# Performance work log

Hardware: AMD Instinct MI355X
Metric: run time of the kernel (lower is better)

Reference implementation:

```python
import jax, jax.numpy as jnp
import numpy as np

PATCH = 16       # patch_size
HALF = 8         # patch_size // 2
SEARCH_HALF = 20 # search_size // 2
NCAND = 40       # candidates per axis (stride=1)
WIN = NCAND + PATCH  # 56: search window side
NUM_PATCHES = 256
IMG_RES = 256    # hard-coded in `patch_ids * H // 256`
EPS = 1e-7


def setup_inputs() -> dict:
    key = jax.random.key(0)
    k0, k1, k2, k3, k4 = jax.random.split(key, 5)
    feat0 = jax.random.normal(k0, (1, 3, 256, 256), jnp.float32)
    feat1 = jax.random.normal(k1, (1, 256, 256, 256), jnp.float32)
    feat2 = jax.random.normal(k2, (1, 512, 128, 128), jnp.float32)
    feat3 = jax.random.normal(k3, (1, 1024, 64, 64), jnp.float32)
    # interior location so the 40x40 candidate grid is full (static shape)
    sample_loc = jax.random.randint(k4, (2,), 28, 228, dtype=jnp.int32)
    return {"feat0": feat0, "feat1": feat1, "feat2": feat2,
            "feat3": feat3, "sample_loc": sample_loc}


def _l2norm(x):
    # Normalize(power=2): x / (sqrt(sum(x^2, dim=1)) + 1e-7)
    norm = jnp.sqrt(jnp.sum(x * x, axis=1, keepdims=True))
    return x / (norm + EPS)


def _select_patch_ids(img, sample_loc):
    # brute-force SSD search of 16x16 patches in a 40x40 stride-1 grid
    C = img.shape[1]
    lh, lw = sample_loc[0], sample_loc[1]
    window = jax.lax.dynamic_slice(
        img, (0, 0, lh - SEARCH_HALF - HALF, lw - SEARCH_HALF - HALF),
        (1, C, WIN, WIN))[0]                       # [C,56,56]
    idx = jnp.arange(NCAND)[:, None] + jnp.arange(PATCH)[None, :]  # [40,16]
    # all candidate patches: [C,40,40,16,16]
    patches = window[:, idx[:, None, :, None], idx[None, :, None, :]]
    sample = jax.lax.dynamic_slice(
        img, (0, 0, lh - HALF, lw - HALF), (1, C, PATCH, PATCH))[0]  # [C,16,16]
    diff = patches - sample[:, None, None, :, :]
    dist = jnp.sqrt(jnp.sum(diff * diff, axis=(0, 3, 4)))  # [40,40] L2 distance
    # topk smallest, sorted ascending
    _, top_idx = jax.lax.top_k(-dist.reshape(-1), NUM_PATCHES)
    hs = lh - SEARCH_HALF + jnp.arange(NCAND)
    ws = lw - SEARCH_HALF + jnp.arange(NCAND)
    locs = jnp.stack(jnp.meshgrid(hs, ws, indexing='ij'), axis=-1).reshape(-1, 2)
    return locs[top_idx].astype(jnp.int32)  # [256,2]


def _gather_norm(feat, patch_ids):
    B, C, H, W = feat.shape
    feat_reshape = feat.transpose(0, 2, 3, 1).reshape(B, H * W, C)
    feat_patch_loc = (patch_ids * H) // IMG_RES          # floor_divide
    patch_id = feat_patch_loc[:, 0] * W + feat_patch_loc[:, 1]
    x_sample = feat_reshape[:, patch_id, :].reshape(-1, C)  # [B*256, C]
    return _l2norm(x_sample)


def reference(feat0, feat1, feat2, feat3, sample_loc):
    patch_ids = _select_patch_ids(feat0, sample_loc)
    outs = tuple(_gather_norm(f, patch_ids) for f in (feat0, feat1, feat2, feat3))
    return (*outs, patch_ids)
```

## Files before the change

### kernel.cpp

```cpp
#include <hip/hip_runtime.h>

#define NCAND 40
#define NC2   1600
#define NP    256

__global__ void k_dist(const float* __restrict__ feat0,
                       const int* __restrict__ loc,
                       float* __restrict__ dist) {
    __shared__ float smp[3 * 16 * 16];
    const int lh = loc[0], lw = loc[1];
    for (int t = threadIdx.x; t < 768; t += 256) {
        int c = t >> 8;
        int rem = t & 255;
        int a = rem >> 4;
        int b = rem & 15;
        smp[t] = feat0[c * 65536 + (lh - 8 + a) * 256 + (lw - 8 + b)];
    }
    __syncthreads();

    const int wid  = threadIdx.x >> 6;
    const int lane = threadIdx.x & 63;
    const int cand = blockIdx.x * 4 + wid;
    const int i = cand / NCAND;
    const int j = cand % NCAND;
    const int base_h = lh - 28 + i;
    const int base_w = lw - 28 + j;

    int c = lane >> 4;
    if (c > 2) c = 0;
    const int h = (lane >> 3) & 1;
    const int u = lane & 7;
    const float* fp = feat0 + c * 65536;
    const float* sc = smp + c * 256;

    float r = 0.0f;
#pragma unroll
    for (int k = 0; k < 16; ++k) {
        const int idx = h * 128 + k * 8 + u;
        const int a = idx >> 4;
        const int b = idx & 15;
        float v = fp[(base_h + a) * 256 + base_w + b];
        float d = __fsub_rn(v, sc[idx]);
        float sq = __fmul_rn(d, d);
        r = (k == 0) ? sq : __fadd_rn(r, sq);
    }
    r = __fadd_rn(r, __shfl_xor(r, 1, 64));
    r = __fadd_rn(r, __shfl_xor(r, 2, 64));
    r = __fadd_rn(r, __shfl_xor(r, 4, 64));
    r = __fadd_rn(r, __shfl_xor(r, 8, 64));
    float p1 = __shfl(r, 16, 64);
    float p2 = __shfl(r, 32, 64);
    float tot = __fadd_rn(__fadd_rn(r, p1), p2);
    if (lane == 0) dist[cand] = __fsqrt_rn(tot);
}

template <int C, int H>
__device__ __forceinline__ void wave_gather(const float* __restrict__ src,
                                            long off, int r, int h, int w,
                                            int lane, float* __restrict__ out) {
    const int hh = (h * H) / 256;
    const int ww = (w * H) / 256;
    const long HW = (long)H * H;
    const long base = (long)hh * H + ww;

    float x[(C + 63) / 64];
    float acc = 0.f;
#pragma unroll
    for (int m = 0; m < (C + 63) / 64; ++m) {
        const int c = lane + m * 64;
        float v = (c < C) ? src[(long)c * HW + base] : 0.f;
        x[m] = v;
        acc = fmaf(v, v, acc);
    }
    acc += __shfl_xor(acc, 1, 64);
    acc += __shfl_xor(acc, 2, 64);
    acc += __shfl_xor(acc, 4, 64);
    acc += __shfl_xor(acc, 8, 64);
    acc += __shfl_xor(acc, 16, 64);
    acc += __shfl_xor(acc, 32, 64);
    const float scale = 1.0f / (sqrtf(acc) + 1e-7f);
#pragma unroll
    for (int m = 0; m < (C + 63) / 64; ++m) {
        const int c = lane + m * 64;
        if (c < C) out[off + (long)r * C + c] = x[m] * scale;
    }
}

__global__ void k_rankgather(const float* __restrict__ dist,
                             const int* __restrict__ loc,
                             const float* __restrict__ feat0,
                             const float* __restrict__ feat1,
                             const float* __restrict__ feat2,
                             const float* __restrict__ feat3,
                             float* __restrict__ out) {
    __shared__ float ds[NC2];
    for (int k = threadIdx.x; k < NC2; k += 256) ds[k] = dist[k];
    __syncthreads();

    const int wid  = threadIdx.x >> 6;
    const int lane = threadIdx.x & 63;
    const int t = blockIdx.x * 4 + wid;
    const float dt = ds[t];
    int rank = 0;
#pragma unroll
    for (int m = 0; m < NC2 / 64; ++m) {
        const int k = lane + (m << 6);
        const float dk = ds[k];
        rank += (dk < dt || (dk == dt && k < t)) ? 1 : 0;
    }
    rank += __shfl_xor(rank, 1, 64);
    rank += __shfl_xor(rank, 2, 64);
    rank += __shfl_xor(rank, 4, 64);
    rank += __shfl_xor(rank, 8, 64);
    rank += __shfl_xor(rank, 16, 64);
    rank += __shfl_xor(rank, 32, 64);

    if (rank < NP) {
        const int lh = loc[0], lw = loc[1];
        const int h = lh - 20 + t / NCAND;
        const int w = lw - 20 + t % NCAND;
        if (lane == 0) {
            float* out_ids = out + 768 + 65536 + 131072 + 262144;
            out_ids[rank * 2]     = (float)h;
            out_ids[rank * 2 + 1] = (float)w;
        }
        wave_gather<3,    256>(feat0, 0,                      rank, h, w, lane, out);
        wave_gather<256,  256>(feat1, 768,                    rank, h, w, lane, out);
        wave_gather<512,  128>(feat2, 768 + 65536,            rank, h, w, lane, out);
        wave_gather<1024, 64 >(feat3, 768 + 65536 + 131072,   rank, h, w, lane, out);
    }
}

extern "C" void kernel_launch(void* const* d_in, const int* in_sizes, int n_in,
                              void* d_out, int out_size, void* d_ws, size_t ws_size,
                              hipStream_t stream) {
    const float* feat0 = (const float*)d_in[0];
    const float* feat1 = (const float*)d_in[1];
    const float* feat2 = (const float*)d_in[2];
    const float* feat3 = (const float*)d_in[3];
    const int*   loc   = (const int*)d_in[4];
    float* out = (float*)d_out;

    float* dist = (float*)d_ws;

    k_dist<<<NC2 / 4, 256, 0, stream>>>(feat0, loc, dist);
    k_rankgather<<<NC2 / 4, 256, 0, stream>>>(dist, loc, feat0, feat1, feat2, feat3, out);
}
```

Baseline: 19.80 us.

## Prefetch feature gathers speculatively before rank computation and drop shared-memory staging

In the rank-and-gather kernel, each wave now issues its gather loads for all four feature maps, plus the distance values, straight into registers before computing the candidate's rank. Before, those loads waited until the rank test passed. The shared-memory staging and barriers are removed from both kernels, and the sample patch is read directly from global memory. This overlaps the gather latency with the rank reduction, at the cost of roughly six times as many gathers, since all 1600 candidates load even though only 256 are kept, and higher register pressure.

```diff
diff --git a/kernel.cpp b/kernel.cpp
--- a/kernel.cpp
+++ b/kernel.cpp
@@ -7,19 +7,9 @@
 __global__ void k_dist(const float* __restrict__ feat0,
                        const int* __restrict__ loc,
                        float* __restrict__ dist) {
-    __shared__ float smp[3 * 16 * 16];
-    const int lh = loc[0], lw = loc[1];
-    for (int t = threadIdx.x; t < 768; t += 256) {
-        int c = t >> 8;
-        int rem = t & 255;
-        int a = rem >> 4;
-        int b = rem & 15;
-        smp[t] = feat0[c * 65536 + (lh - 8 + a) * 256 + (lw - 8 + b)];
-    }
-    __syncthreads();
-
     const int wid  = threadIdx.x >> 6;
     const int lane = threadIdx.x & 63;
+    const int lh = loc[0], lw = loc[1];
     const int cand = blockIdx.x * 4 + wid;
     const int i = cand / NCAND;
     const int j = cand % NCAND;
@@ -31,16 +21,20 @@
     const int h = (lane >> 3) & 1;
     const int u = lane & 7;
     const float* fp = feat0 + c * 65536;
-    const float* sc = smp + c * 256;
 
-    float r = 0.0f;
+    float v[16], s[16];
 #pragma unroll
     for (int k = 0; k < 16; ++k) {
         const int idx = h * 128 + k * 8 + u;
         const int a = idx >> 4;
         const int b = idx & 15;
-        float v = fp[(base_h + a) * 256 + base_w + b];
-        float d = __fsub_rn(v, sc[idx]);
+        v[k] = fp[(base_h + a) * 256 + base_w + b];
+        s[k] = fp[(lh - 8 + a) * 256 + (lw - 8 + b)];
+    }
+    float r = 0.0f;
+#pragma unroll
+    for (int k = 0; k < 16; ++k) {
+        float d = __fsub_rn(v[k], s[k]);
         float sq = __fmul_rn(d, d);
         r = (k == 0) ? sq : __fadd_rn(r, sq);
     }
@@ -55,23 +49,27 @@
 }
 
 template <int C, int H>
-__device__ __forceinline__ void wave_gather(const float* __restrict__ src,
-                                            long off, int r, int h, int w,
-                                            int lane, float* __restrict__ out) {
+__device__ __forceinline__ void gather_load(const float* __restrict__ src,
+                                            int h, int w, int lane,
+                                            float* __restrict__ x) {
     const int hh = (h * H) / 256;
     const int ww = (w * H) / 256;
     const long HW = (long)H * H;
     const long base = (long)hh * H + ww;
-
-    float x[(C + 63) / 64];
-    float acc = 0.f;
 #pragma unroll
     for (int m = 0; m < (C + 63) / 64; ++m) {
         const int c = lane + m * 64;
-        float v = (c < C) ? src[(long)c * HW + base] : 0.f;
-        x[m] = v;
-        acc = fmaf(v, v, acc);
+        x[m] = (c < C) ? src[(long)c * HW + base] : 0.f;
     }
+}
+
+template <int C>
+__device__ __forceinline__ void gather_store(const float* __restrict__ x,
+                                             long off, int r, int lane,
+                                             float* __restrict__ out) {
+    float acc = 0.f;
+#pragma unroll
+    for (int m = 0; m < (C + 63) / 64; ++m) acc = fmaf(x[m], x[m], acc);
     acc += __shfl_xor(acc, 1, 64);
     acc += __shfl_xor(acc, 2, 64);
     acc += __shfl_xor(acc, 4, 64);
@@ -93,20 +91,29 @@
                              const float* __restrict__ feat2,
                              const float* __restrict__ feat3,
                              float* __restrict__ out) {
-    __shared__ float ds[NC2];
-    for (int k = threadIdx.x; k < NC2; k += 256) ds[k] = dist[k];
-    __syncthreads();
-
     const int wid  = threadIdx.x >> 6;
     const int lane = threadIdx.x & 63;
     const int t = blockIdx.x * 4 + wid;
-    const float dt = ds[t];
+    const int lh = loc[0], lw = loc[1];
+    const int h = lh - 20 + t / NCAND;
+    const int w = lw - 20 + t % NCAND;
+
+    const float dt = dist[t];
+    float dk[NC2 / 64];
+#pragma unroll
+    for (int m = 0; m < NC2 / 64; ++m) dk[m] = dist[lane + (m << 6)];
+
+    float x0[1], x1[4], x2[8], x3[16];
+    gather_load<3,    256>(feat0, h, w, lane, x0);
+    gather_load<256,  256>(feat1, h, w, lane, x1);
+    gather_load<512,  128>(feat2, h, w, lane, x2);
+    gather_load<1024, 64 >(feat3, h, w, lane, x3);
+
     int rank = 0;
 #pragma unroll
     for (int m = 0; m < NC2 / 64; ++m) {
         const int k = lane + (m << 6);
-        const float dk = ds[k];
-        rank += (dk < dt || (dk == dt && k < t)) ? 1 : 0;
+        rank += (dk[m] < dt || (dk[m] == dt && k < t)) ? 1 : 0;
     }
     rank += __shfl_xor(rank, 1, 64);
     rank += __shfl_xor(rank, 2, 64);
@@ -116,18 +123,15 @@
     rank += __shfl_xor(rank, 32, 64);
 
     if (rank < NP) {
-        const int lh = loc[0], lw = loc[1];
-        const int h = lh - 20 + t / NCAND;
-        const int w = lw - 20 + t % NCAND;
         if (lane == 0) {
             float* out_ids = out + 768 + 65536 + 131072 + 262144;
             out_ids[rank * 2]     = (float)h;
             out_ids[rank * 2 + 1] = (float)w;
         }
-        wave_gather<3,    256>(feat0, 0,                      rank, h, w, lane, out);
-        wave_gather<256,  256>(feat1, 768,                    rank, h, w, lane, out);
-        wave_gather<512,  128>(feat2, 768 + 65536,            rank, h, w, lane, out);
-        wave_gather<1024, 64 >(feat3, 768 + 65536 + 131072,   rank, h, w, lane, out);
+        gather_store<3   >(x0, 0,                       rank, lane, out);
+        gather_store<256 >(x1, 768,                     rank, lane, out);
+        gather_store<512 >(x2, 768 + 65536,             rank, lane, out);
+        gather_store<1024>(x3, 768 + 65536 + 131072,    rank, lane, out);
     }
 }
 
```

After: 18.34 us. -7.4%, faster.
